# Kernel tuning notes

Hardware: AMD Instinct MI355X
Metric: run time of the kernel (lower is better)

Reference implementation:

```python
import jax, jax.numpy as jnp
import numpy as np

B = 32; LS = 512; LABEL = 256; PRED = 256; LD = 512   # LD = LS//2 + PRED
CIN = 21; COUT = 21; D = 512; H = 8; E = 64; M = 64   # M = top frequency modes
DFF = 2048; LE = 2; MARK = 4; K = 25; EPS = 1e-5


def moving_mean(x):
    # series_decomp moving average: edge-replicate pad then window mean (via cumsum)
    p = (K - 1) // 2
    xp = jnp.pad(x, ((0, 0), (p, p), (0, 0)), mode='edge')
    c = jnp.cumsum(xp, axis=1)
    c = jnp.concatenate([jnp.zeros_like(c[:, :1]), c], axis=1)
    return (c[:, K:] - c[:, :-K]) / K


def decomp(x):
    m = moving_mean(x)
    return x - m, m   # (high/seasonal, low/trend)


def circ_conv(x, k):  # x [B,L,C], k [3,C,O], kernel-3 circular conv, no bias
    xp = jnp.pad(x, ((0, 0), (1, 1), (0, 0)), mode='wrap')
    return jax.lax.conv_general_dilated(xp, k, (1,), 'VALID', dimension_numbers=('NWC', 'WIO', 'NWC'))


def embed(x, mark, ck, tw):  # DataEmbedding_wo_pos: token conv + timeF linear
    return circ_conv(x, ck) + mark @ tw


def heads(x):  # [B,L,D] -> [B,L,H,E]
    return x.reshape(x.shape[0], x.shape[1], H, E)


def freq_self(q, wre, wim):  # FrequencyAdaptiveAttention; q [B,L,H,E]
    L = q.shape[1]
    x = jnp.transpose(q, (0, 2, 3, 1))            # [B,H,E,L]
    xf = jnp.fft.rfft(x, axis=-1)                 # [B,H,E,Lf]
    amp = jnp.mean(jnp.abs(xf), axis=(0, 1, 2))   # adaptive mode selection
    _, idx = jax.lax.top_k(amp, M)
    xs = xf[..., idx]                             # [B,H,E,M]
    w = (wre + 1j * wim).astype(xs.dtype)         # [H,E,E,M] complex
    outs = jnp.einsum('bhem,heom->bhom', xs, w)
    oft = jnp.zeros(xf.shape, xf.dtype).at[..., idx].set(outs)
    y = jnp.fft.irfft(oft, n=L, axis=-1)
    return jnp.transpose(y, (0, 3, 1, 2))         # [B,L,H,E]


def freq_cross(q, k, wre, wim):  # AlignmentFrequencyAttention
    Lq = q.shape[1]
    qf = jnp.fft.rfft(jnp.transpose(q, (0, 2, 3, 1)), axis=-1)
    kf = jnp.fft.rfft(jnp.transpose(k, (0, 2, 3, 1)), axis=-1)
    _, qi = jax.lax.top_k(jnp.mean(jnp.abs(qf), axis=(0, 1, 2)), M)
    _, ki = jax.lax.top_k(jnp.mean(jnp.abs(kf), axis=(0, 1, 2)), M)
    qs = qf[..., qi]; ks = kf[..., ki]            # [B,H,E,M]
    qk = jnp.tanh(jnp.einsum('bhex,bhey->bhxy', qs, ks))
    qkv = jnp.einsum('bhxy,bhey->bhex', qk, ks)
    w = (wre + 1j * wim).astype(qs.dtype)
    outs = jnp.einsum('bhex,heox->bhox', qkv, w)
    oft = jnp.zeros(qf.shape, qf.dtype).at[..., qi].set(outs)
    y = jnp.fft.irfft(oft / (D * D), n=Lq, axis=-1)
    return jnp.transpose(y, (0, 3, 1, 2))


def my_layernorm(x, g, b):  # LN then subtract time-mean (Autoformer my_Layernorm)
    mu = jnp.mean(x, -1, keepdims=True)
    var = jnp.var(x, -1, keepdims=True)
    xh = (x - mu) * jax.lax.rsqrt(var + EPS) * g + b
    return xh - jnp.mean(xh, axis=1, keepdims=True)


def _forward(x_enc, x_mark_enc, x_dec, x_mark_dec, emb_enc_k, emb_enc_t, emb_dec_k, emb_dec_t, fw_enc_re, fw_enc_im, fw_dec_re, fw_dec_im, fw_cr_re, fw_cr_im, enc_Wq, enc_bq, enc_Wo, enc_bo, enc_c1, enc_c2, enc_ng, enc_nb, ds_Wq, ds_bq, ds_Wo, ds_bo, dc_Wq, dc_bq, dc_Wk, dc_bk, dc_Wo, dc_bo, dec_c1, dec_c2, dec_tp, dec_ng, dec_nb, proj_W, proj_b):
    mean = jnp.broadcast_to(jnp.mean(x_enc, axis=1, keepdims=True), (B, PRED, CIN))
    high_init, low_init = decomp(x_enc)
    low_init = jnp.concatenate([low_init[:, -LABEL:, :], mean], axis=1)       # [B,LD,CIN]
    high_init = jnp.pad(high_init[:, -LABEL:, :], ((0, 0), (0, PRED), (0, 0)))
    # encoder
    enc = embed(x_enc, x_mark_enc, emb_enc_k, emb_enc_t)                      # [B,LS,D]
    for i in range(LE):
        a = freq_self(heads(enc @ enc_Wq[i] + enc_bq[i]), fw_enc_re, fw_enc_im)
        a = a.reshape(B, LS, D) @ enc_Wo[i] + enc_bo[i]
        x1, _ = decomp(enc + a)
        y = jax.nn.gelu(x1 @ enc_c1[i]) @ enc_c2[i]
        enc, _ = decomp(x1 + y)
    enc = my_layernorm(enc, enc_ng, enc_nb)
    # decoder (1 layer)
    dec = embed(high_init, x_mark_dec, emb_dec_k, emb_dec_t)                  # [B,LD,D]
    a = freq_self(heads(dec @ ds_Wq + ds_bq), fw_dec_re, fw_dec_im)
    a = a.reshape(B, LD, D) @ ds_Wo + ds_bo
    x1, t1 = decomp(dec + a)
    c = freq_cross(heads(x1 @ dc_Wq + dc_bq), heads(enc @ dc_Wk + dc_bk), fw_cr_re, fw_cr_im)
    c = c.reshape(B, LD, D) @ dc_Wo + dc_bo
    x2, t2 = decomp(x1 + c)
    y = jax.nn.gelu(x2 @ dec_c1) @ dec_c2
    x3, t3 = decomp(x2 + y)
    low_part = low_init + circ_conv(t1 + t2 + t3, dec_tp)                     # trend branch
    high_part = my_layernorm(x3, dec_ng, dec_nb) @ proj_W + proj_b            # seasonal branch
    return (low_part + high_part)[:, -PRED:, :]


def setup_inputs():
    key = jax.random.key(0)
    ks = jax.random.split(key, 32)
    r = lambda i, shape, s=1.0: jax.random.normal(ks[i], shape, dtype=jnp.float32) * s
    z = lambda shape: jnp.zeros(shape, jnp.float32)
    sd = D ** -0.5
    return {
        'x_enc': r(0, (B, LS, CIN)), 'x_mark_enc': r(1, (B, LS, MARK)),
        'x_dec': r(2, (B, LD, CIN)), 'x_mark_dec': r(3, (B, LD, MARK)),
        'emb_enc_k': r(4, (3, CIN, D), 0.1), 'emb_enc_t': r(5, (MARK, D), 0.1),
        'emb_dec_k': r(6, (3, CIN, D), 0.1), 'emb_dec_t': r(7, (MARK, D), 0.1),
        'fw_enc_re': r(8, (H, E, E, M), 0.02), 'fw_enc_im': r(9, (H, E, E, M), 0.02),
        'fw_dec_re': r(10, (H, E, E, M), 0.02), 'fw_dec_im': r(11, (H, E, E, M), 0.02),
        'fw_cr_re': r(12, (H, E, E, M), 0.02), 'fw_cr_im': r(13, (H, E, E, M), 0.02),
        'enc_Wq': r(14, (LE, D, D), sd), 'enc_bq': z((LE, D)),
        'enc_Wo': r(15, (LE, D, D), sd), 'enc_bo': z((LE, D)),
        'enc_c1': r(16, (LE, D, DFF), sd), 'enc_c2': r(17, (LE, DFF, D), DFF ** -0.5),
        'enc_ng': jnp.ones((D,), jnp.float32), 'enc_nb': z((D,)),
        'ds_Wq': r(18, (D, D), sd), 'ds_bq': z((D,)),
        'ds_Wo': r(19, (D, D), sd), 'ds_bo': z((D,)),
        'dc_Wq': r(20, (D, D), sd), 'dc_bq': z((D,)),
        'dc_Wk': r(21, (D, D), sd), 'dc_bk': z((D,)),
        'dc_Wo': r(22, (D, D), sd), 'dc_bo': z((D,)),
        'dec_c1': r(23, (D, DFF), sd), 'dec_c2': r(24, (DFF, D), DFF ** -0.5),
        'dec_tp': r(25, (3, D, COUT), sd),
        'dec_ng': jnp.ones((D,), jnp.float32), 'dec_nb': z((D,)),
        'proj_W': r(26, (D, COUT), sd), 'proj_b': z((COUT,)),
    }


def reference(x_enc, x_mark_enc, x_dec, x_mark_dec, emb_enc_k, emb_enc_t, emb_dec_k, emb_dec_t, fw_enc_re, fw_enc_im, fw_dec_re, fw_dec_im, fw_cr_re, fw_cr_im, enc_Wq, enc_bq, enc_Wo, enc_bo, enc_c1, enc_c2, enc_ng, enc_nb, ds_Wq, ds_bq, ds_Wo, ds_bo, dc_Wq, dc_bq, dc_Wk, dc_bk, dc_Wo, dc_bo, dec_c1, dec_c2, dec_tp, dec_ng, dec_nb, proj_W, proj_b):
    return _forward(x_enc, x_mark_enc, x_dec, x_mark_dec, emb_enc_k, emb_enc_t, emb_dec_k, emb_dec_t, fw_enc_re, fw_enc_im, fw_dec_re, fw_dec_im, fw_cr_re, fw_cr_im, enc_Wq, enc_bq, enc_Wo, enc_bo, enc_c1, enc_c2, enc_ng, enc_nb, ds_Wq, ds_bq, ds_Wo, ds_bo, dc_Wq, dc_bq, dc_Wk, dc_bk, dc_Wo, dc_bo, dec_c1, dec_c2, dec_tp, dec_ng, dec_nb, proj_W, proj_b)
```

## Files before the change

### kernel.cpp

```cpp
#include <hip/hip_runtime.h>
#include <math.h>

#define B_    32
#define LQ    512
#define CIN_  21
#define COUT_ 21
#define D_    512
#define H_    8
#define E_    64
#define M_    64
#define DFF_  2048
#define MARK_ 4
#define KWIN  25
#define PW    12
#define LF    257
#define TW    320
#define PRED_ 256
#define EPS_  1e-5f
#define SPECH (16384 * 256)

static __device__ __forceinline__ int iclamp(int v, int lo, int hi) {
  return v < lo ? lo : (v > hi ? hi : v);
}

__global__ void k_dft_tables(float* __restrict__ cosF, float* __restrict__ negsinF,
                             float* __restrict__ c512, float* __restrict__ s512) {
  int i = blockIdx.x * 256 + threadIdx.x;
  if (i < 512) {
    float th = (float)i * (6.283185307179586f / 512.0f);
    c512[i] = cosf(th);
    s512[i] = sinf(th);
  }
  if (i >= 512 * TW) return;
  int t = i / TW, f = i % TW;
  if (f >= LF) { cosF[i] = 0.f; negsinF[i] = 0.f; return; }
  int r = (t * f) & 511;
  float th = (float)r * (6.283185307179586f / 512.0f);
  cosF[i] = cosf(th);
  negsinF[i] = -sinf(th);
}

__global__ void k_enc_decomp(const float* __restrict__ x,
                             float* __restrict__ lowi, float* __restrict__ highi) {
  int b = blockIdx.x, c = threadIdx.x;
  if (c >= CIN_) return;
  const float* xb = x + (long)b * LQ * CIN_ + c;
  float s = 0.f;
  for (int t = 0; t < LQ; t++) s += xb[(long)t * CIN_];
  float mean = s / (float)LQ;
  for (int t = 256; t < LQ; t++) {
    float w = 0.f;
    for (int j = t - PW; j <= t + PW; j++) {
      int jj = iclamp(j, 0, LQ - 1);
      w += xb[(long)jj * CIN_];
    }
    float m = w * (1.f / KWIN);
    lowi [((long)b * LQ + (t - 256)) * CIN_ + c] = m;
    highi[((long)b * LQ + (t - 256)) * CIN_ + c] = xb[(long)t * CIN_] - m;
  }
  for (int t = 256; t < LQ; t++) {
    lowi [((long)b * LQ + t) * CIN_ + c] = mean;
    highi[((long)b * LQ + t) * CIN_ + c] = 0.f;
  }
}

__global__ void k_embed(const float* __restrict__ x, const float* __restrict__ mark,
                        const float* __restrict__ ck, const float* __restrict__ tw,
                        float* __restrict__ out) {
  int o = blockIdx.x * 256 + threadIdx.x;
  int t = blockIdx.y, b = blockIdx.z;
  float acc = 0.f;
  const float* xb = x + (long)b * LQ * CIN_;
  #pragma unroll
  for (int j = 0; j < 3; j++) {
    int tt = (t + j - 1 + LQ) & (LQ - 1);
    const float* xr = xb + (long)tt * CIN_;
    const float* kr = ck + (long)(j * CIN_) * D_ + o;
    for (int c = 0; c < CIN_; c++) acc = fmaf(xr[c], kr[(long)c * D_], acc);
  }
  const float* mr = mark + ((long)b * LQ + t) * MARK_;
  #pragma unroll
  for (int mm = 0; mm < MARK_; mm++) acc = fmaf(mr[mm], tw[(long)mm * D_ + o], acc);
  out[((long)b * LQ + t) * D_ + o] = acc;
}

template<int ACT>
__global__ __launch_bounds__(256) void k_gemm(
    const float* __restrict__ A, const float* __restrict__ Bm,
    const float* __restrict__ bias, float* __restrict__ C,
    int Mr, int Nd, int Kd) {
  constexpr int BM = 128, BN = 128, BK = 32, SA = BM + 1;
  __shared__ float As[BK][SA];
  __shared__ float Bs[BK][BN];
  int m0 = blockIdx.y * BM, n0 = blockIdx.x * BN;
  int tid = threadIdx.x;
  int tx = tid & 15, ty = tid >> 4;
  float acc[8][8] = {};
  const float* Ag = A + (long)m0 * Kd;
  for (int k0 = 0; k0 < Kd; k0 += BK) {
    #pragma unroll
    for (int r = 0; r < 4; r++) {
      int slot = tid + r * 256;
      int row = slot >> 3, k4 = slot & 7;
      const float4 v = *(const float4*)&Ag[(long)row * Kd + k0 + k4 * 4];
      As[k4 * 4 + 0][row] = v.x; As[k4 * 4 + 1][row] = v.y;
      As[k4 * 4 + 2][row] = v.z; As[k4 * 4 + 3][row] = v.w;
    }
    #pragma unroll
    for (int r = 0; r < 4; r++) {
      int slot = tid + r * 256;
      int kk = slot >> 5, n4 = slot & 31;
      *(float4*)&Bs[kk][n4 * 4] = *(const float4*)&Bm[(long)(k0 + kk) * Nd + n0 + n4 * 4];
    }
    __syncthreads();
    #pragma unroll
    for (int kk = 0; kk < BK; kk++) {
      float av[8], bv[8];
      #pragma unroll
      for (int i = 0; i < 8; i++) av[i] = As[kk][ty * 8 + i];
      #pragma unroll
      for (int j = 0; j < 8; j++) bv[j] = Bs[kk][tx * 8 + j];
      #pragma unroll
      for (int i = 0; i < 8; i++)
        #pragma unroll
        for (int j = 0; j < 8; j++)
          acc[i][j] = fmaf(av[i], bv[j], acc[i][j]);
    }
    __syncthreads();
  }
  float bj[8];
  #pragma unroll
  for (int j = 0; j < 8; j++) bj[j] = bias ? bias[n0 + tx * 8 + j] : 0.f;
  #pragma unroll
  for (int i = 0; i < 8; i++) {
    long gm = m0 + ty * 8 + i;
    float* Crow = C + gm * Nd + n0 + tx * 8;
    #pragma unroll
    for (int j4 = 0; j4 < 2; j4++) {
      float4 v;
      float t0[4];
      #pragma unroll
      for (int j = 0; j < 4; j++) {
        float x = acc[i][j4 * 4 + j] + bj[j4 * 4 + j];
        if (ACT == 1) {
          float x3 = x * x * x;
          float th = tanhf(0.7978845608028654f * (x + 0.044715f * x3));
          x = 0.5f * x * (1.f + th);
        }
        t0[j] = x;
      }
      v.x = t0[0]; v.y = t0[1]; v.z = t0[2]; v.w = t0[3];
      *(float4*)&Crow[j4 * 4] = v;
    }
  }
}

__global__ void k_zero(float* __restrict__ p, int n) {
  int i = blockIdx.x * 256 + threadIdx.x;
  if (i < n) p[i] = 0.f;
}

__global__ __launch_bounds__(256) void k_dftamp(
    const float* __restrict__ X, const float* __restrict__ cosP,
    const float* __restrict__ nsinP, float* __restrict__ specR,
    float* __restrict__ specI, float* __restrict__ nyqR,
    float* __restrict__ nyqI, float* __restrict__ amp) {
  constexpr int BK = 32;
  __shared__ float As[BK][132];
  __shared__ float Cs[BK][68];
  __shared__ float Ss[BK][68];
  int m0 = blockIdx.x * 128;
  int n0 = blockIdx.y * 64;
  int tid = threadIdx.x, tx = tid & 15, ty = tid >> 4;
  int b = m0 >> 9, d0 = m0 & 511;
  const float* Xb = X + (long)b * LQ * D_ + d0;
  float aR[8][4] = {}, aI[8][4] = {};
  for (int k0 = 0; k0 < 512; k0 += BK) {
    #pragma unroll
    for (int r = 0; r < 4; r++) {
      int slot = tid + r * 256;
      int kk = slot >> 5, d4 = slot & 31;
      *(float4*)&As[kk][d4 * 4] = *(const float4*)&Xb[(long)(k0 + kk) * D_ + d4 * 4];
    }
    #pragma unroll
    for (int r = 0; r < 2; r++) {
      int slot = tid + r * 256;
      int kk = slot >> 4, f4 = slot & 15;
      *(float4*)&Cs[kk][f4 * 4] = *(const float4*)&cosP [(long)(k0 + kk) * TW + n0 + f4 * 4];
      *(float4*)&Ss[kk][f4 * 4] = *(const float4*)&nsinP[(long)(k0 + kk) * TW + n0 + f4 * 4];
    }
    __syncthreads();
    #pragma unroll
    for (int kk = 0; kk < BK; kk++) {
      float av[8], cv[4], sv[4];
      *(float4*)&av[0] = *(const float4*)&As[kk][ty * 8];
      *(float4*)&av[4] = *(const float4*)&As[kk][ty * 8 + 4];
      *(float4*)&cv[0] = *(const float4*)&Cs[kk][tx * 4];
      *(float4*)&sv[0] = *(const float4*)&Ss[kk][tx * 4];
      #pragma unroll
      for (int i = 0; i < 8; i++)
        #pragma unroll
        for (int j = 0; j < 4; j++) {
          aR[i][j] = fmaf(av[i], cv[j], aR[i][j]);
          aI[i][j] = fmaf(av[i], sv[j], aI[i][j]);
        }
    }
    __syncthreads();
  }
  int c0 = n0 + tx * 4;
  #pragma unroll
  for (int i = 0; i < 8; i++) {
    long row = m0 + ty * 8 + i;
    if (c0 < 256) {
      *(float4*)&specR[row * 256 + c0] = make_float4(aR[i][0], aR[i][1], aR[i][2], aR[i][3]);
      *(float4*)&specI[row * 256 + c0] = make_float4(aI[i][0], aI[i][1], aI[i][2], aI[i][3]);
    } else if (c0 == 256) {
      nyqR[row] = aR[i][0];
      nyqI[row] = aI[i][0];
    }
  }
  __shared__ float csum[16][68];
  #pragma unroll
  for (int j = 0; j < 4; j++) {
    float s = 0.f;
    #pragma unroll
    for (int i = 0; i < 8; i++)
      s += sqrtf(aR[i][j] * aR[i][j] + aI[i][j] * aI[i][j]);
    csum[ty][tx * 4 + j] = s;
  }
  __syncthreads();
  if (tid < 64) {
    float s = 0.f;
    #pragma unroll
    for (int r = 0; r < 16; r++) s += csum[r][tid];
    if (n0 + tid < LF) atomicAdd(&amp[n0 + tid], s);
  }
}

__global__ void k_topk(const float* __restrict__ amp, int* __restrict__ idx) {
  __shared__ float v[512];
  __shared__ float rv[512];
  __shared__ int   ri[512];
  int tid = threadIdx.x;
  v[tid] = (tid < LF) ? amp[tid] : -INFINITY;
  __syncthreads();
  for (int k = 0; k < M_; k++) {
    rv[tid] = v[tid]; ri[tid] = tid;
    __syncthreads();
    for (int st = 256; st > 0; st >>= 1) {
      if (tid < st) {
        float a = rv[tid], b = rv[tid + st];
        int ai = ri[tid], bi = ri[tid + st];
        if (b > a || (b == a && bi < ai)) { rv[tid] = b; ri[tid] = bi; }
      }
      __syncthreads();
    }
    if (tid == 0) { idx[k] = ri[0]; v[ri[0]] = -INFINITY; }
    __syncthreads();
  }
}

__global__ void k_gathercols(const float* __restrict__ specR, const float* __restrict__ specI,
                             const float* __restrict__ nyqR, const float* __restrict__ nyqI,
                             const int* __restrict__ idx,
                             float* __restrict__ gR, float* __restrict__ gI) {
  int tid = threadIdx.x;
  int m = tid & 63, r = tid >> 6;
  long row = (long)blockIdx.x * 4 + r;
  int f = idx[m];
  long o = row * 64 + m;
  if (f < 256) { gR[o] = specR[row * 256 + f]; gI[o] = specI[row * 256 + f]; }
  else         { gR[o] = nyqR[row];            gI[o] = nyqI[row]; }
}

__global__ __launch_bounds__(256) void k_modemix(
    const float* __restrict__ sre, const float* __restrict__ sim,
    const float* __restrict__ wre, const float* __restrict__ wim,
    float* __restrict__ ore, float* __restrict__ oim) {
  int b = blockIdx.z, h = blockIdx.y, oc = blockIdx.x;
  int m = threadIdx.x, osub = threadIdx.y;
  int o = oc * 4 + osub;
  __shared__ float xr[E_][M_], xi[E_][M_];
  #pragma unroll
  for (int r = 0; r < 16; r++) {
    int e = r * 4 + osub;
    long a = ((long)(b * H_ + h) * E_ + e) * M_ + m;
    xr[e][m] = sre[a]; xi[e][m] = sim[a];
  }
  __syncthreads();
  float ar = 0.f, ai = 0.f;
  const float* wrb = wre + ((long)(h * E_) * E_ + o) * M_ + m;
  const float* wib = wim + ((long)(h * E_) * E_ + o) * M_ + m;
  #pragma unroll 4
  for (int e = 0; e < E_; e++) {
    float wr = wrb[(long)e * E_ * M_], wi = wib[(long)e * E_ * M_];
    float qr = xr[e][m], qi = xi[e][m];
    ar = fmaf(qr, wr, ar); ar = fmaf(-qi, wi, ar);
    ai = fmaf(qr, wi, ai); ai = fmaf(qi, wr, ai);
  }
  long oaddr = ((long)(b * H_ + h) * E_ + o) * M_ + m;
  ore[oaddr] = ar; oim[oaddr] = ai;
}

__global__ __launch_bounds__(512) void k_irfft(
    const float* __restrict__ ore, const float* __restrict__ oim,
    const int* __restrict__ idx, const float* __restrict__ c512,
    const float* __restrict__ s512, float scale, float* __restrict__ out) {
  int d = blockIdx.x, b = blockIdx.y, t = threadIdx.x;
  int h = d >> 6, o = d & 63;
  __shared__ float mr[M_], mi[M_];
  __shared__ int   mf[M_];
  __shared__ float cs[512], sn[512];
  cs[t] = c512[t]; sn[t] = s512[t];
  if (t < M_) {
    long a = ((long)(b * H_ + h) * E_ + o) * M_ + t;
    int f = idx[t];
    mf[t] = f;
    float c = (f == 0 || f == 256) ? 1.f : 2.f;
    mr[t] = ore[a] * c; mi[t] = oim[a] * c;
  }
  __syncthreads();
  float acc = 0.f;
  #pragma unroll 8
  for (int m = 0; m < M_; m++) {
    int r = (mf[m] * t) & 511;
    acc += mr[m] * cs[r] - mi[m] * sn[r];
  }
  out[((long)b * LQ + t) * D_ + d] = acc * scale;
}

__global__ void k_decomp(const float* __restrict__ a, const float* __restrict__ bsrc,
                         float* __restrict__ season, float* __restrict__ trend,
                         int trendMode) {
  int c = blockIdx.x * 256 + threadIdx.x;
  int t0 = blockIdx.y * 64;
  int b = blockIdx.z;
  long base = (long)b * LQ * D_ + c;
  float s = 0.f;
  for (int j = t0 - PW; j <= t0 + PW; j++) {
    int tt = iclamp(j, 0, LQ - 1);
    float v = a[base + (long)tt * D_];
    if (bsrc) v += bsrc[base + (long)tt * D_];
    s += v;
  }
  for (int t = t0; t < t0 + 64; t++) {
    float cur = a[base + (long)t * D_];
    if (bsrc) cur += bsrc[base + (long)t * D_];
    float m = s * (1.f / KWIN);
    season[base + (long)t * D_] = cur - m;
    if (trendMode == 1) trend[base + (long)t * D_] = m;
    else if (trendMode == 2) trend[base + (long)t * D_] += m;
    int tn = iclamp(t + PW + 1, 0, LQ - 1), to = iclamp(t - PW, 0, LQ - 1);
    float vn = a[base + (long)tn * D_], vo = a[base + (long)to * D_];
    if (bsrc) { vn += bsrc[base + (long)tn * D_]; vo += bsrc[base + (long)to * D_]; }
    s += vn - vo;
  }
}

__global__ __launch_bounds__(256) void k_ln(const float* __restrict__ x,
                                            const float* __restrict__ g,
                                            const float* __restrict__ bt,
                                            float* __restrict__ out) {
  long row = blockIdx.x;
  const float* xr = x + row * D_;
  float v1 = xr[threadIdx.x], v2 = xr[threadIdx.x + 256];
  __shared__ float rs[256], rq[256];
  rs[threadIdx.x] = v1 + v2;
  rq[threadIdx.x] = v1 * v1 + v2 * v2;
  __syncthreads();
  for (int st = 128; st > 0; st >>= 1) {
    if (threadIdx.x < st) { rs[threadIdx.x] += rs[threadIdx.x + st]; rq[threadIdx.x] += rq[threadIdx.x + st]; }
    __syncthreads();
  }
  float mu = rs[0] / (float)D_;
  float var = fmaxf(rq[0] / (float)D_ - mu * mu, 0.f);
  float inv = rsqrtf(var + EPS_);
  out[row * D_ + threadIdx.x]       = (v1 - mu) * inv * g[threadIdx.x]       + bt[threadIdx.x];
  out[row * D_ + threadIdx.x + 256] = (v2 - mu) * inv * g[threadIdx.x + 256] + bt[threadIdx.x + 256];
}

__global__ void k_tmsub(const float* __restrict__ x, float* __restrict__ out) {
  int dcol = blockIdx.x * 256 + threadIdx.x, b = blockIdx.y;
  long base = (long)b * LQ * D_ + dcol;
  float s = 0.f;
  for (int t = 0; t < LQ; t++) s += x[base + (long)t * D_];
  float mu = s / (float)LQ;
  for (int t = 0; t < LQ; t++) out[base + (long)t * D_] = x[base + (long)t * D_] - mu;
}

__global__ __launch_bounds__(256) void k_qk(
    const float* __restrict__ qR, const float* __restrict__ qI,
    const float* __restrict__ kR, const float* __restrict__ kI,
    float* __restrict__ qkre, float* __restrict__ qkim) {
  int b = blockIdx.z, h = blockIdx.y, xc = blockIdx.x;
  int y = threadIdx.x, xs4 = threadIdx.y;
  __shared__ float ksr[E_][64], ksi[E_][64];
  __shared__ float qsr[E_][16], qsi[E_][16];
  long base = (long)(b * H_ + h) * E_;
  int tid = threadIdx.y * 64 + threadIdx.x;
  #pragma unroll
  for (int r = 0; r < 16; r++) {
    int e = r * 4 + xs4;
    long a = (base + e) * 64 + y;
    ksr[e][y] = kR[a]; ksi[e][y] = kI[a];
  }
  #pragma unroll
  for (int r = 0; r < 4; r++) {
    int ii = tid + r * 256;
    int e = ii >> 4, xl = ii & 15;
    long a = (base + e) * 64 + xc * 16 + xl;
    qsr[e][xl] = qR[a]; qsi[e][xl] = qI[a];
  }
  __syncthreads();
  #pragma unroll
  for (int xi = 0; xi < 4; xi++) {
    int xl = xs4 * 4 + xi;
    float ar = 0.f, ai = 0.f;
    for (int e = 0; e < E_; e++) {
      float a1 = qsr[e][xl], b1 = qsi[e][xl], c1 = ksr[e][y], d1 = ksi[e][y];
      ar += a1 * c1 - b1 * d1;
      ai += a1 * d1 + b1 * c1;
    }
    float s = tanhf(ar), t = tanf(ai);
    float t2 = t * t;
    float den = 1.f + s * s * t2;
    float outr = s * (1.f + t2) / den;
    float outi = t * (1.f - s * s) / den;
    int x = xc * 16 + xl;
    long oa = ((long)(b * H_ + h) * M_ + y) * M_ + x;
    qkre[oa] = outr; qkim[oa] = outi;
  }
}

__global__ __launch_bounds__(256) void k_qkv(
    const float* __restrict__ qkre, const float* __restrict__ qkim,
    const float* __restrict__ kR, const float* __restrict__ kI,
    float* __restrict__ vre, float* __restrict__ vim) {
  int b = blockIdx.z, h = blockIdx.y, ec = blockIdx.x;
  int x = threadIdx.x, es = threadIdx.y;
  int e = ec * 4 + es;
  __shared__ float qr[M_][M_], qi2[M_][M_];
  int tid = threadIdx.y * 64 + threadIdx.x;
  #pragma unroll
  for (int r = 0; r < 16; r++) {
    int ii = tid + r * 256;
    int yy = ii >> 6, xx = ii & 63;
    long a = ((long)(b * H_ + h) * M_ + yy) * M_ + xx;
    qr[yy][xx] = qkre[a]; qi2[yy][xx] = qkim[a];
  }
  __syncthreads();
  float ar = 0.f, ai = 0.f;
  long kbase = ((long)(b * H_ + h) * E_ + e) * 64;
  for (int y = 0; y < M_; y++) {
    float c1 = kR[kbase + y], d1 = kI[kbase + y];
    float a1 = qr[y][x], b1 = qi2[y][x];
    ar += a1 * c1 - b1 * d1;
    ai += a1 * d1 + b1 * c1;
  }
  long o = ((long)(b * H_ + h) * E_ + e) * M_ + x;
  vre[o] = ar; vim[o] = ai;
}

__global__ __launch_bounds__(256) void k_final(
    const float* __restrict__ lowi, const float* __restrict__ tsum,
    const float* __restrict__ tp, const float* __restrict__ ln3,
    const float* __restrict__ projW, const float* __restrict__ projb,
    float* __restrict__ out) {
  int o = threadIdx.x;
  int rowi = blockIdx.x * 8 + threadIdx.y;
  int b = rowi >> 8, tpi = rowi & 255;
  int t = tpi + 256;
  if (o >= COUT_) return;
  float acc = lowi[((long)b * LQ + t) * CIN_ + o] + projb[o];
  #pragma unroll
  for (int j = 0; j < 3; j++) {
    int tt = (t + j - 1 + LQ) & (LQ - 1);
    const float* xr = tsum + ((long)b * LQ + tt) * D_;
    const float* kr = tp + (long)(j * D_) * COUT_ + o;
    for (int c = 0; c < D_; c++) acc = fmaf(xr[c], kr[(long)c * COUT_], acc);
  }
  const float* lr = ln3 + ((long)b * LQ + t) * D_;
  for (int d0 = 0; d0 < D_; d0++) acc = fmaf(lr[d0], projW[(long)d0 * COUT_ + o], acc);
  out[((long)b * PRED_ + tpi) * COUT_ + o] = acc;
}

extern "C" void kernel_launch(void* const* d_in, const int* in_sizes, int n_in,
                              void* d_out, int out_size, void* d_ws, size_t ws_size,
                              hipStream_t stream) {
  const float* x_enc      = (const float*)d_in[0];
  const float* x_mark_enc = (const float*)d_in[1];
  const float* x_mark_dec = (const float*)d_in[3];
  const float* emb_enc_k  = (const float*)d_in[4];
  const float* emb_enc_t  = (const float*)d_in[5];
  const float* emb_dec_k  = (const float*)d_in[6];
  const float* emb_dec_t  = (const float*)d_in[7];
  const float* fw_enc_re  = (const float*)d_in[8];
  const float* fw_enc_im  = (const float*)d_in[9];
  const float* fw_dec_re  = (const float*)d_in[10];
  const float* fw_dec_im  = (const float*)d_in[11];
  const float* fw_cr_re   = (const float*)d_in[12];
  const float* fw_cr_im   = (const float*)d_in[13];
  const float* enc_Wq     = (const float*)d_in[14];
  const float* enc_bq     = (const float*)d_in[15];
  const float* enc_Wo     = (const float*)d_in[16];
  const float* enc_bo     = (const float*)d_in[17];
  const float* enc_c1     = (const float*)d_in[18];
  const float* enc_c2     = (const float*)d_in[19];
  const float* enc_ng     = (const float*)d_in[20];
  const float* enc_nb     = (const float*)d_in[21];
  const float* ds_Wq      = (const float*)d_in[22];
  const float* ds_bq      = (const float*)d_in[23];
  const float* ds_Wo      = (const float*)d_in[24];
  const float* ds_bo      = (const float*)d_in[25];
  const float* dc_Wq      = (const float*)d_in[26];
  const float* dc_bq      = (const float*)d_in[27];
  const float* dc_Wk      = (const float*)d_in[28];
  const float* dc_bk      = (const float*)d_in[29];
  const float* dc_Wo      = (const float*)d_in[30];
  const float* dc_bo      = (const float*)d_in[31];
  const float* dec_c1     = (const float*)d_in[32];
  const float* dec_c2     = (const float*)d_in[33];
  const float* dec_tp     = (const float*)d_in[34];
  const float* dec_ng     = (const float*)d_in[35];
  const float* dec_nb     = (const float*)d_in[36];
  const float* proj_W     = (const float*)d_in[37];
  const float* proj_b     = (const float*)d_in[38];
  float* out = (float*)d_out;
  float* ws  = (float*)d_ws;

  constexpr size_t BIG = (size_t)B_ * LQ * D_;
  constexpr size_t OUS = (size_t)B_ * H_ * E_ * M_;
  size_t o = 0;
  auto nxt = [&](size_t n) { size_t r = o; o += (n + 255) & ~(size_t)255; return r; };
  size_t oA = nxt(BIG), oB = nxt(BIG), oC = nxt(BIG), oTS = nxt(BIG);
  size_t oQSR = nxt(OUS), oQSI = nxt(OUS), oKSR = nxt(OUS), oKSI = nxt(OUS),
         oOR = nxt(OUS), oOI = nxt(OUS), oQKR = nxt(OUS), oQKI = nxt(OUS);
  size_t oCOS = nxt((size_t)512 * TW), oNSN = nxt((size_t)512 * TW);
  size_t oC5 = nxt(512), oS5 = nxt(512);
  size_t oAMP = nxt(512), oIQ = nxt(64), oIK = nxt(64);
  size_t oNR = nxt(16384), oNI = nxt(16384);
  size_t oLOW = nxt((size_t)B_ * LQ * CIN_), oHI = nxt((size_t)B_ * LQ * CIN_);
  size_t oFF = nxt(0);
  int FCH = 2048;
  if ((oFF + (size_t)16384 * DFF_) * 4 <= ws_size)      FCH = 16384;
  else if ((oFF + (size_t)4096 * DFF_) * 4 <= ws_size)  FCH = 4096;
  (void)in_sizes; (void)n_in; (void)out_size;

  int* idxq = (int*)(ws + oIQ);
  int* idxk = (int*)(ws + oIK);

  auto GEMM = [&](const float* Ap, const float* Bp, const float* bias,
                  float* Cp, int Mr, int Nd, int Kd, int act) {
    dim3 g(Nd / 128, Mr / 128, 1);
    if (act) k_gemm<1><<<g, dim3(256), 0, stream>>>(Ap, Bp, bias, Cp, Mr, Nd, Kd);
    else     k_gemm<0><<<g, dim3(256), 0, stream>>>(Ap, Bp, bias, Cp, Mr, Nd, Kd);
  };
  auto AMPSEL = [&](const float* x, float* scratch, int* idxp) {
    k_zero<<<2, 256, 0, stream>>>(ws + oAMP, 512);
    k_dftamp<<<dim3(128, 5), 256, 0, stream>>>(x, ws + oCOS, ws + oNSN,
        scratch, scratch + SPECH, ws + oNR, ws + oNI, ws + oAMP);
    k_topk<<<1, 512, 0, stream>>>(ws + oAMP, idxp);
  };
  auto GATHER = [&](const float* scratch, const int* idxp, float* gR, float* gI) {
    k_gathercols<<<4096, 256, 0, stream>>>(scratch, scratch + SPECH,
        ws + oNR, ws + oNI, idxp, gR, gI);
  };
  auto MODEMIX = [&](const float* sR, const float* sI, const float* wre, const float* wim) {
    k_modemix<<<dim3(16, H_, B_), dim3(64, 4), 0, stream>>>(sR, sI, wre, wim, ws + oOR, ws + oOI);
  };
  auto IRFFT = [&](const int* idxp, float scale, float* dst) {
    k_irfft<<<dim3(D_, B_), 512, 0, stream>>>(ws + oOR, ws + oOI, idxp,
                                              ws + oC5, ws + oS5, scale, dst);
  };
  auto DECOMP = [&](const float* a, const float* bsrc, float* season, float* trend, int mode) {
    k_decomp<<<dim3(D_ / 256, LQ / 64, B_), 256, 0, stream>>>(a, bsrc, season, trend, mode);
  };
  auto FFNP = [&](const float* x, const float* c1, const float* c2, float* y) {
    for (int ch = 0; ch < (B_ * LQ) / FCH; ch++) {
      GEMM(x + (size_t)ch * FCH * D_, c1, nullptr, ws + oFF, FCH, DFF_, D_, 1);
      GEMM(ws + oFF, c2, nullptr, y + (size_t)ch * FCH * D_, FCH, D_, DFF_, 0);
    }
  };

  k_dft_tables<<<(512 * TW + 255) / 256, 256, 0, stream>>>(ws + oCOS, ws + oNSN,
                                                           ws + oC5, ws + oS5);
  k_enc_decomp<<<B_, 32, 0, stream>>>(x_enc, ws + oLOW, ws + oHI);
  k_embed<<<dim3(2, LQ, B_), 256, 0, stream>>>(x_enc, x_mark_enc, emb_enc_k, emb_enc_t, ws + oA);

  for (int i = 0; i < 2; i++) {
    GEMM(ws + oA, enc_Wq + (size_t)i * D_ * D_, enc_bq + (size_t)i * D_, ws + oB, B_ * LQ, D_, D_, 0);
    AMPSEL(ws + oB, ws + oC, idxq);
    GATHER(ws + oC, idxq, ws + oQSR, ws + oQSI);
    MODEMIX(ws + oQSR, ws + oQSI, fw_enc_re, fw_enc_im);
    IRFFT(idxq, 1.f / 512.f, ws + oB);
    GEMM(ws + oB, enc_Wo + (size_t)i * D_ * D_, enc_bo + (size_t)i * D_, ws + oC, B_ * LQ, D_, D_, 0);
    DECOMP(ws + oA, ws + oC, ws + oB, nullptr, 0);
    FFNP(ws + oB, enc_c1 + (size_t)i * D_ * DFF_, enc_c2 + (size_t)i * DFF_ * D_, ws + oC);
    DECOMP(ws + oB, ws + oC, ws + oA, nullptr, 0);
  }
  k_ln<<<B_ * LQ, 256, 0, stream>>>(ws + oA, enc_ng, enc_nb, ws + oB);
  k_tmsub<<<dim3(2, B_), 256, 0, stream>>>(ws + oB, ws + oA);

  GEMM(ws + oA, dc_Wk, dc_bk, ws + oB, B_ * LQ, D_, D_, 0);
  AMPSEL(ws + oB, ws + oC, idxk);
  GATHER(ws + oC, idxk, ws + oKSR, ws + oKSI);

  k_embed<<<dim3(2, LQ, B_), 256, 0, stream>>>(ws + oHI, x_mark_dec, emb_dec_k, emb_dec_t, ws + oA);
  GEMM(ws + oA, ds_Wq, ds_bq, ws + oB, B_ * LQ, D_, D_, 0);
  AMPSEL(ws + oB, ws + oC, idxq);
  GATHER(ws + oC, idxq, ws + oQSR, ws + oQSI);
  MODEMIX(ws + oQSR, ws + oQSI, fw_dec_re, fw_dec_im);
  IRFFT(idxq, 1.f / 512.f, ws + oB);
  GEMM(ws + oB, ds_Wo, ds_bo, ws + oC, B_ * LQ, D_, D_, 0);
  DECOMP(ws + oA, ws + oC, ws + oB, ws + oTS, 1);

  GEMM(ws + oB, dc_Wq, dc_bq, ws + oC, B_ * LQ, D_, D_, 0);
  AMPSEL(ws + oC, ws + oA, idxq);
  GATHER(ws + oA, idxq, ws + oQSR, ws + oQSI);
  k_qk<<<dim3(4, H_, B_), dim3(64, 4), 0, stream>>>(
      ws + oQSR, ws + oQSI, ws + oKSR, ws + oKSI, ws + oQKR, ws + oQKI);
  k_qkv<<<dim3(16, H_, B_), dim3(64, 4), 0, stream>>>(
      ws + oQKR, ws + oQKI, ws + oKSR, ws + oKSI, ws + oQSR, ws + oQSI);
  MODEMIX(ws + oQSR, ws + oQSI, fw_cr_re, fw_cr_im);
  IRFFT(idxq, 1.f / (512.f * 262144.f), ws + oC);
  GEMM(ws + oC, dc_Wo, dc_bo, ws + oA, B_ * LQ, D_, D_, 0);
  DECOMP(ws + oB, ws + oA, ws + oC, ws + oTS, 2);
  FFNP(ws + oC, dec_c1, dec_c2, ws + oA);
  DECOMP(ws + oC, ws + oA, ws + oB, ws + oTS, 2);
  k_ln<<<B_ * LQ, 256, 0, stream>>>(ws + oB, dec_ng, dec_nb, ws + oA);
  k_tmsub<<<dim3(2, B_), 256, 0, stream>>>(ws + oA, ws + oC);
  k_final<<<dim3(B_ * PRED_ / 8), dim3(32, 8), 0, stream>>>(
      ws + oLOW, ws + oTS, dec_tp, ws + oC, proj_W, proj_b, out);
}
```

Measured before the change: 9.075 ms.

## Prefetch GEMM tiles into registers and split thread tiles to avoid LDS conflicts

The FP32 GEMM kernel now loads the next K-tile from global memory into registers while it computes on the current shared-memory tile, hiding global load latency behind the FMAs. Each thread's 8x8 output is split into two 4-wide halves 64 apart, so B reads become float4 loads with fewer LDS bank conflicts. Workgroup indices are also remapped across 8 groups, apparently to match the chiplet layout for better L2 locality. The cost is extra registers for the prefetch buffers, which could reduce occupancy.

```diff
diff --git a/kernel.cpp b/kernel.cpp
--- a/kernel.cpp
+++ b/kernel.cpp
@@ -92,56 +92,96 @@
   constexpr int BM = 128, BN = 128, BK = 32, SA = BM + 1;
   __shared__ float As[BK][SA];
   __shared__ float Bs[BK][BN];
-  int m0 = blockIdx.y * BM, n0 = blockIdx.x * BN;
+  int nwg = gridDim.x * gridDim.y;
+  int wg = blockIdx.y * gridDim.x + blockIdx.x;
+  if ((nwg & 7) == 0) {
+    int cpx = nwg >> 3;
+    wg = (wg & 7) * cpx + (wg >> 3);
+  }
+  int bx = wg % gridDim.x, by = wg / gridDim.x;
+  int m0 = by * BM, n0 = bx * BN;
   int tid = threadIdx.x;
   int tx = tid & 15, ty = tid >> 4;
   float acc[8][8] = {};
   const float* Ag = A + (long)m0 * Kd;
-  for (int k0 = 0; k0 < Kd; k0 += BK) {
+  float4 ra[4], rb[4];
+
+  auto loadG = [&](int k0) {
     #pragma unroll
     for (int r = 0; r < 4; r++) {
       int slot = tid + r * 256;
       int row = slot >> 3, k4 = slot & 7;
-      const float4 v = *(const float4*)&Ag[(long)row * Kd + k0 + k4 * 4];
-      As[k4 * 4 + 0][row] = v.x; As[k4 * 4 + 1][row] = v.y;
-      As[k4 * 4 + 2][row] = v.z; As[k4 * 4 + 3][row] = v.w;
+      ra[r] = *(const float4*)&Ag[(long)row * Kd + k0 + k4 * 4];
     }
     #pragma unroll
     for (int r = 0; r < 4; r++) {
       int slot = tid + r * 256;
       int kk = slot >> 5, n4 = slot & 31;
-      *(float4*)&Bs[kk][n4 * 4] = *(const float4*)&Bm[(long)(k0 + kk) * Nd + n0 + n4 * 4];
-    }
-    __syncthreads();
+      rb[r] = *(const float4*)&Bm[(long)(k0 + kk) * Nd + n0 + n4 * 4];
+    }
+  };
+  auto storeL = [&]() {
+    #pragma unroll
+    for (int r = 0; r < 4; r++) {
+      int slot = tid + r * 256;
+      int row = slot >> 3, k4 = slot & 7;
+      As[k4 * 4 + 0][row] = ra[r].x; As[k4 * 4 + 1][row] = ra[r].y;
+      As[k4 * 4 + 2][row] = ra[r].z; As[k4 * 4 + 3][row] = ra[r].w;
+    }
+    #pragma unroll
+    for (int r = 0; r < 4; r++) {
+      int slot = tid + r * 256;
+      int kk = slot >> 5, n4 = slot & 31;
+      *(float4*)&Bs[kk][n4 * 4] = rb[r];
+    }
+  };
+  auto compute = [&]() {
     #pragma unroll
     for (int kk = 0; kk < BK; kk++) {
       float av[8], bv[8];
       #pragma unroll
-      for (int i = 0; i < 8; i++) av[i] = As[kk][ty * 8 + i];
-      #pragma unroll
-      for (int j = 0; j < 8; j++) bv[j] = Bs[kk][tx * 8 + j];
+      for (int i = 0; i < 4; i++) {
+        av[i]     = As[kk][ty * 4 + i];
+        av[i + 4] = As[kk][64 + ty * 4 + i];
+      }
+      *(float4*)&bv[0] = *(const float4*)&Bs[kk][tx * 4];
+      *(float4*)&bv[4] = *(const float4*)&Bs[kk][64 + tx * 4];
       #pragma unroll
       for (int i = 0; i < 8; i++)
         #pragma unroll
         for (int j = 0; j < 8; j++)
           acc[i][j] = fmaf(av[i], bv[j], acc[i][j]);
     }
+  };
+
+  loadG(0);
+  storeL();
+  __syncthreads();
+  for (int k0 = BK; k0 < Kd; k0 += BK) {
+    loadG(k0);
+    compute();
     __syncthreads();
-  }
+    storeL();
+    __syncthreads();
+  }
+  compute();
+
   float bj[8];
   #pragma unroll
-  for (int j = 0; j < 8; j++) bj[j] = bias ? bias[n0 + tx * 8 + j] : 0.f;
+  for (int j = 0; j < 4; j++) {
+    bj[j]     = bias ? bias[n0 + tx * 4 + j]      : 0.f;
+    bj[j + 4] = bias ? bias[n0 + 64 + tx * 4 + j] : 0.f;
+  }
   #pragma unroll
   for (int i = 0; i < 8; i++) {
-    long gm = m0 + ty * 8 + i;
-    float* Crow = C + gm * Nd + n0 + tx * 8;
-    #pragma unroll
-    for (int j4 = 0; j4 < 2; j4++) {
-      float4 v;
+    long gm = m0 + (i < 4 ? ty * 4 + i : 64 + ty * 4 + (i - 4));
+    float* Crow = C + gm * Nd + n0;
+    #pragma unroll
+    for (int half = 0; half < 2; half++) {
       float t0[4];
       #pragma unroll
       for (int j = 0; j < 4; j++) {
-        float x = acc[i][j4 * 4 + j] + bj[j4 * 4 + j];
+        float x = acc[i][half * 4 + j] + bj[half * 4 + j];
         if (ACT == 1) {
           float x3 = x * x * x;
           float th = tanhf(0.7978845608028654f * (x + 0.044715f * x3));
@@ -149,8 +189,7 @@
         }
         t0[j] = x;
       }
-      v.x = t0[0]; v.y = t0[1]; v.z = t0[2]; v.w = t0[3];
-      *(float4*)&Crow[j4 * 4] = v;
+      *(float4*)&Crow[half * 64 + tx * 4] = make_float4(t0[0], t0[1], t0[2], t0[3]);
     }
   }
 }
```

Result: slower. 13.40 ms (+47.7%).
